# Optimization experiments

Measured on AMD Instinct MI355X. Metric: run time of the kernel, lower is better.

Reference implementation:

```python
import jax, jax.numpy as jnp
import numpy as np

N_SIN = 3  # fcn_n_sin

def _feats(x):
    # x: [B, Din] -> features [B, Din, 1 + 2*N_SIN]
    omega = (2.0 ** jnp.arange(N_SIN, dtype=x.dtype))  # [n_sin]
    ox = x[..., None] * omega  # [B, Din, n_sin]
    return jnp.concatenate([x[..., None], jnp.sin(ox), jnp.cos(ox)], axis=-1)

def setup_inputs() -> dict:
    key = jax.random.key(0)
    k1, k2, k3 = jax.random.split(key, 3)
    B, Din, Dout, H, F = 2048, 64, 64, 32, 1 + 2 * N_SIN
    x = jax.random.normal(k1, (B, Din), dtype=jnp.float32)
    # xavier-normal-ish init for W1/W2, zeros for biases (matches init_parameters)
    W1 = jax.random.normal(k2, (Din, Dout, H, F), dtype=jnp.float32) * np.sqrt(2.0 / (H + F))
    W2 = jax.random.normal(k3, (Din, Dout, 1, H), dtype=jnp.float32) * np.sqrt(2.0 / (1 + H))
    B1 = jnp.zeros((Din, Dout, H), dtype=jnp.float32)
    B2 = jnp.zeros((Din, Dout, 1), dtype=jnp.float32)
    return {"x": x, "W1": W1, "W2": W2, "B1": B1, "B2": B2}

def reference(x, W1, W2, B1, B2):
    f = _feats(x)  # [B, Din, F]
    # per-edge first layer: [B, Din, Dout, H]
    h = jnp.einsum('bif,iohf->bioh', f, W1) + B1[None]
    h = jax.nn.silu(h)
    # per-edge second layer -> scalar: [B, Din, Dout]
    phis = jnp.einsum('bioh,ioh->bio', h, W2[:, :, 0, :]) + B2[:, :, 0][None]
    return phis.sum(axis=1)  # [B, Dout]
```

## Files before the change

### kernel.cpp

```cpp
#include <hip/hip_runtime.h>
#include <math.h>

typedef _Float16 f16;
typedef f16   f16x8    __attribute__((ext_vector_type(8)));
typedef float floatx4  __attribute__((ext_vector_type(4)));
typedef float floatx16 __attribute__((ext_vector_type(16)));

#define LOG2E 1.44269504088896340736f

#define B_SZ  2048
#define DIN   64
#define DOUT  64
#define NH    32

#define NIG   4
#define IGW   (DIN / NIG)

#define W1IMG_ELEMS ((size_t)DIN * DOUT * 64 * 8)
#define FIMG_ELEMS  ((size_t)DIN * 64 * 64 * 8)
#define W2Q_ELEMS   ((size_t)DIN * DOUT * NH)

__global__ __launch_bounds__(256) void prep_kernel(
        const float* __restrict__ W1, const float* __restrict__ B1,
        const float* __restrict__ W2, const float* __restrict__ B2,
        const float* __restrict__ x,
        f16* __restrict__ w1img, f16* __restrict__ fimg,
        float* __restrict__ w2q, float* __restrict__ b2sum) {
    const int bid = blockIdx.x, tid = threadIdx.x;
    if (bid < 1024) {
        int e = bid * 256 + tid;
        int lane = e & 63, o = (e >> 6) & 63, i = e >> 12;
        f16x8 v = {};
        if (lane < 32) {
            const float* w = W1 + (size_t)((i * 64 + o) * 32 + lane) * 7;
#pragma unroll
            for (int j = 0; j < 7; ++j) v[j] = (f16)(w[j] * (-LOG2E));
            v[7] = (f16)(B1[(i * 64 + o) * 32 + lane] * (-LOG2E));
        }
        *(f16x8*)(w1img + (size_t)e * 8) = v;
    } else if (bid < 2048) {
        int e = (bid - 1024) * 256 + tid;
        int lane = e & 63, btp = (e >> 6) & 63, i = e >> 12;
        f16x8 v = {};
        if (lane < 32) {
            int b = btp * 32 + lane;
            float xv = x[b * 64 + i];
            float s1, c1;
            __sincosf(xv, &s1, &c1);
            float s2 = 2.0f * s1 * c1, c2 = 1.0f - 2.0f * s1 * s1;
            float s4 = 2.0f * s2 * c2, c4 = 1.0f - 2.0f * s2 * s2;
            v[0] = (f16)xv; v[1] = (f16)s1; v[2] = (f16)s2; v[3] = (f16)s4;
            v[4] = (f16)c1; v[5] = (f16)c2; v[6] = (f16)c4; v[7] = (f16)1.0f;
        }
        *(f16x8*)(fimg + (size_t)e * 8) = v;
    } else if (bid < 2560) {
        int e = (bid - 2048) * 256 + tid;
        int r = e & 3, p = (e >> 2) & 1, q = (e >> 3) & 3;
        int o = (e >> 5) & 63, i = e >> 11;
        int h = q * 8 + p * 4 + r;
        w2q[e] = W2[(size_t)(i * 64 + o) * 32 + h] * (-1.0f / LOG2E);
    } else if (tid < 64) {
        float s = 0.0f;
        for (int i = 0; i < 64; ++i) s += B2[i * 64 + tid];
        b2sum[tid] = s;
    }
}

__global__ __launch_bounds__(128, 4) void main_kernel(
        const f16* __restrict__ w1img, const f16* __restrict__ fimg,
        const float* __restrict__ w2q, float* __restrict__ partials) {
    const int tid  = threadIdx.x;
    const int lane = tid & 63;
    const int wv   = tid >> 6;
    const int btp  = blockIdx.x & 63;
    const int og   = (blockIdx.x >> 6) & 31;
    const int ig   = blockIdx.x >> 11;
    const int o    = __builtin_amdgcn_readfirstlane(og * 2 + wv);
    const int p    = lane >> 5;

    const size_t ibase = (size_t)ig * IGW;
    const f16*   ap = w1img + ibase * 32768 + ((size_t)o * 64 + lane) * 8;
    const f16*   bp = fimg  + ibase * 32768 + ((size_t)btp * 64 + lane) * 8;
    const float* wp = w2q   + ibase * 2048  + (size_t)o * 32 + p * 4;

    f16x8 a = *(const f16x8*)ap;
    f16x8 b = *(const f16x8*)bp;
    floatx4 w0 = *(const floatx4*)(wp);
    floatx4 w1 = *(const floatx4*)(wp + 8);
    floatx4 w2 = *(const floatx4*)(wp + 16);
    floatx4 w3 = *(const floatx4*)(wp + 24);

    float phi = 0.0f;
    const floatx16 zeroC = {};

#pragma unroll 1
    for (int ii = 0; ii < IGW; ++ii) {
        const f16x8 ca = a, cb = b;
        const floatx4 cw0 = w0, cw1 = w1, cw2 = w2, cw3 = w3;

        const size_t i1 = (size_t)(ii + 1);
        a  = *(const f16x8*)(ap + i1 * 32768);
        b  = *(const f16x8*)(bp + i1 * 32768);
        w0 = *(const floatx4*)(wp + i1 * 2048);
        w1 = *(const floatx4*)(wp + i1 * 2048 + 8);
        w2 = *(const floatx4*)(wp + i1 * 2048 + 16);
        w3 = *(const floatx4*)(wp + i1 * 2048 + 24);

        floatx16 C = __builtin_amdgcn_mfma_f32_32x32x16_f16(ca, cb, zeroC, 0, 0, 0);

#pragma unroll
        for (int r = 0; r < 4; ++r) {
            float av, e2, sg;
            av = C[0 + r];  e2 = __builtin_amdgcn_exp2f(av);
            sg = __builtin_amdgcn_rcpf(1.0f + e2);
            phi = __builtin_fmaf(av * cw0[r], sg, phi);
            av = C[4 + r];  e2 = __builtin_amdgcn_exp2f(av);
            sg = __builtin_amdgcn_rcpf(1.0f + e2);
            phi = __builtin_fmaf(av * cw1[r], sg, phi);
            av = C[8 + r];  e2 = __builtin_amdgcn_exp2f(av);
            sg = __builtin_amdgcn_rcpf(1.0f + e2);
            phi = __builtin_fmaf(av * cw2[r], sg, phi);
            av = C[12 + r]; e2 = __builtin_amdgcn_exp2f(av);
            sg = __builtin_amdgcn_rcpf(1.0f + e2);
            phi = __builtin_fmaf(av * cw3[r], sg, phi);
        }
    }

    phi += __shfl_xor(phi, 32, 64);

    if (lane < 32) {
        partials[((size_t)ig * B_SZ + btp * 32 + lane) * 64 + o] = phi;
    }
}

__global__ __launch_bounds__(256) void reduce_kernel(
        const float* __restrict__ partials, const float* __restrict__ b2sum,
        float* __restrict__ out) {
    int t = blockIdx.x * 256 + threadIdx.x;
    floatx4 s = *(const floatx4*)(b2sum + ((t * 4) & 63));
#pragma unroll
    for (int gg = 0; gg < NIG; ++gg) {
        floatx4 v = *(const floatx4*)(partials + (size_t)gg * (B_SZ * DOUT) + t * 4);
        s += v;
    }
    *(floatx4*)(out + (size_t)t * 4) = s;
}

extern "C" void kernel_launch(void* const* d_in, const int* in_sizes, int n_in,
                              void* d_out, int out_size, void* d_ws, size_t ws_size,
                              hipStream_t stream) {
    const float* x  = (const float*)d_in[0];
    const float* W1 = (const float*)d_in[1];
    const float* W2 = (const float*)d_in[2];
    const float* B1 = (const float*)d_in[3];
    const float* B2 = (const float*)d_in[4];
    float* out = (float*)d_out;

    f16*   w1img    = (f16*)d_ws;
    f16*   fimg     = w1img + W1IMG_ELEMS;
    float* w2q      = (float*)(fimg + FIMG_ELEMS);
    float* b2sum    = w2q + W2Q_ELEMS;
    float* partials = b2sum + 64;

    prep_kernel<<<2561, 256, 0, stream>>>(W1, B1, W2, B2, x, w1img, fimg, w2q, b2sum);
    main_kernel<<<NIG * 32 * 64, 128, 0, stream>>>(w1img, fimg, w2q, partials);
    reduce_kernel<<<(B_SZ * DOUT) / 1024, 256, 0, stream>>>(partials, b2sum, out);
}
```

Before: 128.9 us.

## Batch sigmoid reciprocals, stage prep through LDS, halve input-dim groups

The inner loop combines four sigmoid terms over a common denominator, so it issues one reciprocal per four activations instead of four. The prep kernel now stages W1/B1 and x tiles through shared memory, which gives coalesced reads and fewer blocks. The number of input-dimension groups drops from 4 to 2, so main has fewer blocks, longer loops and fewer partials to reduce. W2 prefetching is replaced by an in-loop load. The product of four (1+exp2) terms can overflow fp32 for large pre-activations, which could produce inf or NaN.

```diff
diff --git a/kernel.cpp b/kernel.cpp
--- a/kernel.cpp
+++ b/kernel.cpp
@@ -13,7 +13,7 @@
 #define DOUT  64
 #define NH    32
 
-#define NIG   4
+#define NIG   2
 #define IGW   (DIN / NIG)
 
 #define W1IMG_ELEMS ((size_t)DIN * DOUT * 64 * 8)
@@ -27,34 +27,49 @@
         f16* __restrict__ w1img, f16* __restrict__ fimg,
         float* __restrict__ w2q, float* __restrict__ b2sum) {
     const int bid = blockIdx.x, tid = threadIdx.x;
-    if (bid < 1024) {
-        int e = bid * 256 + tid;
-        int lane = e & 63, o = (e >> 6) & 63, i = e >> 12;
-        f16x8 v = {};
-        if (lane < 32) {
-            const float* w = W1 + (size_t)((i * 64 + o) * 32 + lane) * 7;
+    if (bid < 256) {
+        __shared__ float l1[16 * 225];
+        __shared__ float lb[16 * 32];
+        const int base = bid * 16;
+        for (int g = tid; g < 3584; g += 256) {
+            int pair = g / 224, r = g % 224;
+            l1[pair * 225 + r] = W1[(size_t)base * 224 + g];
+        }
+        for (int g = tid; g < 512; g += 256) lb[g] = B1[(size_t)base * 32 + g];
+        __syncthreads();
+        for (int g = tid; g < 1024; g += 256) {
+            int pair = g >> 6, lane = g & 63;
+            f16x8 v = {};
+            if (lane < 32) {
 #pragma unroll
-            for (int j = 0; j < 7; ++j) v[j] = (f16)(w[j] * (-LOG2E));
-            v[7] = (f16)(B1[(i * 64 + o) * 32 + lane] * (-LOG2E));
+                for (int j = 0; j < 7; ++j)
+                    v[j] = (f16)(l1[pair * 225 + lane * 7 + j] * (-LOG2E));
+                v[7] = (f16)(lb[pair * 32 + lane] * (-LOG2E));
+            }
+            *(f16x8*)(w1img + (size_t)bid * 8192 + (size_t)g * 8) = v;
         }
-        *(f16x8*)(w1img + (size_t)e * 8) = v;
-    } else if (bid < 2048) {
-        int e = (bid - 1024) * 256 + tid;
-        int lane = e & 63, btp = (e >> 6) & 63, i = e >> 12;
-        f16x8 v = {};
-        if (lane < 32) {
-            int b = btp * 32 + lane;
-            float xv = x[b * 64 + i];
+    } else if (bid < 320) {
+        __shared__ float ls[32 * 65];
+        const int btp = bid - 256;
+        for (int g = tid; g < 2048; g += 256) {
+            int bb = g >> 6, i = g & 63;
+            ls[bb * 65 + i] = x[(size_t)(btp * 32 + bb) * 64 + i];
+        }
+        __syncthreads();
+        for (int g = tid; g < 2048; g += 256) {
+            int bb = g & 31, i = g >> 5;
+            float xv = ls[bb * 65 + i];
             float s1, c1;
             __sincosf(xv, &s1, &c1);
             float s2 = 2.0f * s1 * c1, c2 = 1.0f - 2.0f * s1 * s1;
             float s4 = 2.0f * s2 * c2, c4 = 1.0f - 2.0f * s2 * s2;
+            f16x8 v;
             v[0] = (f16)xv; v[1] = (f16)s1; v[2] = (f16)s2; v[3] = (f16)s4;
             v[4] = (f16)c1; v[5] = (f16)c2; v[6] = (f16)c4; v[7] = (f16)1.0f;
+            *(f16x8*)(fimg + ((size_t)(i * 64 + btp) * 64 + bb) * 8) = v;
         }
-        *(f16x8*)(fimg + (size_t)e * 8) = v;
-    } else if (bid < 2560) {
-        int e = (bid - 2048) * 256 + tid;
+    } else if (bid < 832) {
+        int e = (bid - 320) * 256 + tid;
         int r = e & 3, p = (e >> 2) & 1, q = (e >> 3) & 3;
         int o = (e >> 5) & 63, i = e >> 11;
         int h = q * 8 + p * 4 + r;
@@ -85,10 +100,6 @@
 
     f16x8 a = *(const f16x8*)ap;
     f16x8 b = *(const f16x8*)bp;
-    floatx4 w0 = *(const floatx4*)(wp);
-    floatx4 w1 = *(const floatx4*)(wp + 8);
-    floatx4 w2 = *(const floatx4*)(wp + 16);
-    floatx4 w3 = *(const floatx4*)(wp + 24);
 
     float phi = 0.0f;
     const floatx16 zeroC = {};
@@ -96,33 +107,35 @@
 #pragma unroll 1
     for (int ii = 0; ii < IGW; ++ii) {
         const f16x8 ca = a, cb = b;
-        const floatx4 cw0 = w0, cw1 = w1, cw2 = w2, cw3 = w3;
 
         const size_t i1 = (size_t)(ii + 1);
-        a  = *(const f16x8*)(ap + i1 * 32768);
-        b  = *(const f16x8*)(bp + i1 * 32768);
-        w0 = *(const floatx4*)(wp + i1 * 2048);
-        w1 = *(const floatx4*)(wp + i1 * 2048 + 8);
-        w2 = *(const floatx4*)(wp + i1 * 2048 + 16);
-        w3 = *(const floatx4*)(wp + i1 * 2048 + 24);
+        a = *(const f16x8*)(ap + i1 * 32768);
+        b = *(const f16x8*)(bp + i1 * 32768);
+
+        const floatx4 w0 = *(const floatx4*)(wp + (size_t)ii * 2048);
+        const floatx4 w1 = *(const floatx4*)(wp + (size_t)ii * 2048 + 8);
+        const floatx4 w2 = *(const floatx4*)(wp + (size_t)ii * 2048 + 16);
+        const floatx4 w3 = *(const floatx4*)(wp + (size_t)ii * 2048 + 24);
 
         floatx16 C = __builtin_amdgcn_mfma_f32_32x32x16_f16(ca, cb, zeroC, 0, 0, 0);
 
 #pragma unroll
-        for (int r = 0; r < 4; ++r) {
-            float av, e2, sg;
-            av = C[0 + r];  e2 = __builtin_amdgcn_exp2f(av);
-            sg = __builtin_amdgcn_rcpf(1.0f + e2);
-            phi = __builtin_fmaf(av * cw0[r], sg, phi);
-            av = C[4 + r];  e2 = __builtin_amdgcn_exp2f(av);
-            sg = __builtin_amdgcn_rcpf(1.0f + e2);
-            phi = __builtin_fmaf(av * cw1[r], sg, phi);
-            av = C[8 + r];  e2 = __builtin_amdgcn_exp2f(av);
-            sg = __builtin_amdgcn_rcpf(1.0f + e2);
-            phi = __builtin_fmaf(av * cw2[r], sg, phi);
-            av = C[12 + r]; e2 = __builtin_amdgcn_exp2f(av);
-            sg = __builtin_amdgcn_rcpf(1.0f + e2);
-            phi = __builtin_fmaf(av * cw3[r], sg, phi);
+        for (int q = 0; q < 4; ++q) {
+            const floatx4 wq = (q == 0) ? w0 : (q == 1) ? w1 : (q == 2) ? w2 : w3;
+            float t0 = C[4 * q + 0], t1 = C[4 * q + 1];
+            float t2 = C[4 * q + 2], t3 = C[4 * q + 3];
+            float u0 = __builtin_amdgcn_exp2f(t0);
+            float u1 = __builtin_amdgcn_exp2f(t1);
+            float u2 = __builtin_amdgcn_exp2f(t2);
+            float u3 = __builtin_amdgcn_exp2f(t3);
+            float v0 = 1.0f + u0, v1 = 1.0f + u1, v2 = 1.0f + u2, v3 = 1.0f + u3;
+            float p0 = t0 * wq[0], p1 = t1 * wq[1], p2 = t2 * wq[2], p3 = t3 * wq[3];
+            float d01 = v0 * v1, d23 = v2 * v3;
+            float n01 = __builtin_fmaf(p1, v0, p0 * v1);
+            float n23 = __builtin_fmaf(p3, v2, p2 * v3);
+            float n   = __builtin_fmaf(n23, d01, n01 * d23);
+            float D   = d01 * d23;
+            phi = __builtin_fmaf(n, __builtin_amdgcn_rcpf(D), phi);
         }
     }
 
@@ -162,7 +175,7 @@
     float* b2sum    = w2q + W2Q_ELEMS;
     float* partials = b2sum + 64;
 
-    prep_kernel<<<2561, 256, 0, stream>>>(W1, B1, W2, B2, x, w1img, fimg, w2q, b2sum);
+    prep_kernel<<<833, 256, 0, stream>>>(W1, B1, W2, B2, x, w1img, fimg, w2q, b2sum);
     main_kernel<<<NIG * 32 * 64, 128, 0, stream>>>(w1img, fimg, w2q, partials);
     reduce_kernel<<<(B_SZ * DOUT) / 1024, 256, 0, stream>>>(partials, b2sum, out);
 }
```

Result: slower. 131.5 us (+2.0%).
